# Kernel tuning notes

Measured on AMD Instinct MI355X. Metric: run time of the kernel, lower is better.

## Reference

```python
import jax, jax.numpy as jnp
import numpy as np

N, NFEAT, K, HK = 500000, 64, 8, 64

def _trunc_normal(key, shape, std):
    # torch.nn.init.trunc_normal_ truncates at +/-2 (then scaled by std)
    return jnp.clip(jax.random.normal(key, shape), -2.0, 2.0) * std

def setup_inputs() -> dict:
    key = jax.random.key(0)
    kx, kz, kt = jax.random.split(key, 3)
    x = jax.random.normal(kx, (N, NFEAT), dtype=jnp.float32)
    # stacked ParameterList: z[i] in R^{h_K x n}, t[i] in R^{h_K}
    z = _trunc_normal(kz, (K, HK, NFEAT), 1.0).astype(jnp.float32)  # b_z = 1.0
    t = _trunc_normal(kt, (K, HK), 1.0).astype(jnp.float32)         # b_t = 1.0
    return {"x": x, "z": z, "t": t}

def reference(x, z, t):
    w = jnp.exp(z)                                  # [K, HK, n], positive weights
    g = jnp.einsum('ni,khi->nkh', x, w) + t         # [N, K, HK]
    max_vals = jnp.max(g, axis=2)                   # [N, K] maxout per group
    max_idx = jnp.argmax(g, axis=2)                 # [N, K]
    y = jnp.min(max_vals, axis=1)                   # [N]   min over groups
    min_idx = jnp.argmin(max_vals, axis=1)          # [N]
    # A[min_idx[n], max_idx[n, min_idx[n]]] += 1  (vectorized scatter-add)
    cols = jnp.take_along_axis(max_idx, min_idx[:, None], axis=1)[:, 0]  # [N]
    A = jnp.zeros((K, HK), dtype=jnp.float32).at[min_idx, cols].add(1.0)
    return y, A
```

## Files before the change

kernel.cpp:

```cpp
#include <hip/hip_runtime.h>
#include <math.h>

constexpr int NS    = 500000;
constexpr int NF    = 64;
constexpr int KG    = 8;
constexpr int HKC   = 64;
constexpr int NCELL = KG * HKC;
constexpr int RPW   = 32;
constexpr int RPB   = 128;
constexpr int NBLK  = (NS + RPB - 1) / RPB;
constexpr int NSLOT = 1954;
constexpr int SLICE = HKC * NF;

typedef __attribute__((ext_vector_type(8))) _Float16 half8;
typedef __attribute__((ext_vector_type(4))) float f32x4;

__device__ __forceinline__ float swz16_f(float v) {
    return __int_as_float(__builtin_amdgcn_ds_swizzle(__float_as_int(v), 0x401F));
}
__device__ __forceinline__ int swz16_i(int v) {
    return __builtin_amdgcn_ds_swizzle(v, 0x401F);
}

__global__ void prep_kernel(const float* __restrict__ z,
                            _Float16* __restrict__ w_hi,
                            _Float16* __restrict__ w_lo,
                            float* __restrict__ A,
                            float4* __restrict__ pzero, int n4) {
    int i = blockIdx.x * blockDim.x + threadIdx.x;
    if (i < KG * HKC * NF) {
        float w = expf(z[i]);
        _Float16 h = (_Float16)w;
        w_hi[i] = h;
        w_lo[i] = (_Float16)(w - (float)h);
    }
    if (i < NCELL) A[i] = 0.0f;
    for (int j = i; j < n4; j += gridDim.x * blockDim.x)
        pzero[j] = (float4){0.f, 0.f, 0.f, 0.f};
}

template <bool PRIV>
__global__ __launch_bounds__(256, 3) void monn_mfma_kernel(
    const float* __restrict__ x,
    const _Float16* __restrict__ w_hi,
    const _Float16* __restrict__ w_lo,
    const float* __restrict__ t,
    float* __restrict__ y,
    float* __restrict__ dest) {

    __shared__ __align__(16) char smem[2 * 8192];
    __shared__ unsigned lhist[NCELL];
    if (PRIV) {
        for (int i = threadIdx.x; i < NCELL; i += 256) lhist[i] = 0u;
    }

    const int tid  = threadIdx.x;
    const int lane = tid & 63;
    const long base  = (long)blockIdx.x * RPB + (tid >> 6) * RPW;
    const bool valid = (base < NS);
    const long cbase = valid ? base : (NS - RPW);
    const int m  = lane & 15;
    const int q  = lane >> 4;
    const int q4 = q * 4;
    const int a32 = ((lane ^ 32) << 2);
    const int x7  = m & 7;
    const int rb0 = m * 128 + (((0 + q) ^ x7) << 4);
    const int rb1 = m * 128 + (((4 + q) ^ x7) << 4);
    const int sr  = tid >> 2;
    const int sc  = (tid & 3) * 2;
    const int sd0 = sr * 128 + (((sc)     ^ (sr & 7)) << 4);
    const int sd1 = sr * 128 + (((sc + 1) ^ (sr & 7)) << 4);

    half8 Xh[2][2], Xl[2][2];
#pragma unroll
    for (int rt = 0; rt < 2; ++rt) {
        const float* xp = x + (cbase + rt * 16 + m) * NF;
#pragma unroll
        for (int s = 0; s < 2; ++s) {
            const int k0 = s * 32 + q * 8;
            const float4 v0 = *reinterpret_cast<const float4*>(xp + k0);
            const float4 v1 = *reinterpret_cast<const float4*>(xp + k0 + 4);
            const float f[8] = {v0.x, v0.y, v0.z, v0.w, v1.x, v1.y, v1.z, v1.w};
#pragma unroll
            for (int j = 0; j < 8; ++j) {
                _Float16 h = (_Float16)f[j];
                Xh[rt][s][j] = h;
                Xl[rt][s][j] = (_Float16)(f[j] - (float)h);
            }
        }
    }

    float ymin[2] = {INFINITY, INFINITY};
    int   code[2] = {0, 0};

#pragma unroll 1
    for (int g = 0; g < KG; ++g) {
        __syncthreads();
        {
            const float4* sh = reinterpret_cast<const float4*>(w_hi + (size_t)g * SLICE);
            const float4* sl = reinterpret_cast<const float4*>(w_lo + (size_t)g * SLICE);
            const float4 h0 = sh[tid * 2], h1 = sh[tid * 2 + 1];
            const float4 l0 = sl[tid * 2], l1 = sl[tid * 2 + 1];
            *reinterpret_cast<float4*>(smem + sd0)        = h0;
            *reinterpret_cast<float4*>(smem + sd1)        = h1;
            *reinterpret_cast<float4*>(smem + 8192 + sd0) = l0;
            *reinterpret_cast<float4*>(smem + 8192 + sd1) = l1;
        }
        __syncthreads();

        f32x4 acc[4][2];
#pragma unroll
        for (int c = 0; c < 4; ++c) {
            const float4 tv = *reinterpret_cast<const float4*>(t + g * HKC + c * 16 + q4);
            const f32x4 tin = (f32x4){tv.x, tv.y, tv.z, tv.w};
            acc[c][0] = tin;
            acc[c][1] = tin;
        }

#pragma unroll
        for (int s = 0; s < 2; ++s) {
            const int rb = s ? rb1 : rb0;
            half8 Wh[4], Wl[4];
#pragma unroll
            for (int c = 0; c < 4; ++c) {
                Wh[c] = *reinterpret_cast<const half8*>(smem + rb + c * 2048);
                Wl[c] = *reinterpret_cast<const half8*>(smem + 8192 + rb + c * 2048);
            }
#pragma unroll
            for (int c = 0; c < 4; ++c)
#pragma unroll
                for (int rt = 0; rt < 2; ++rt)
                    acc[c][rt] = __builtin_amdgcn_mfma_f32_16x16x32_f16(Wh[c], Xh[rt][s], acc[c][rt], 0, 0, 0);
#pragma unroll
            for (int c = 0; c < 4; ++c)
#pragma unroll
                for (int rt = 0; rt < 2; ++rt)
                    acc[c][rt] = __builtin_amdgcn_mfma_f32_16x16x32_f16(Wl[c], Xh[rt][s], acc[c][rt], 0, 0, 0);
#pragma unroll
            for (int c = 0; c < 4; ++c)
#pragma unroll
                for (int rt = 0; rt < 2; ++rt)
                    acc[c][rt] = __builtin_amdgcn_mfma_f32_16x16x32_f16(Wh[c], Xl[rt][s], acc[c][rt], 0, 0, 0);
        }

#pragma unroll
        for (int rt = 0; rt < 2; ++rt) {
            float t01 = fmaxf(acc[0][rt][0], acc[0][rt][1]);
            float t23 = fmaxf(acc[0][rt][2], acc[0][rt][3]);
            float t45 = fmaxf(acc[1][rt][0], acc[1][rt][1]);
            float t67 = fmaxf(acc[1][rt][2], acc[1][rt][3]);
            float t89 = fmaxf(acc[2][rt][0], acc[2][rt][1]);
            float tab = fmaxf(acc[2][rt][2], acc[2][rt][3]);
            float tcd = fmaxf(acc[3][rt][0], acc[3][rt][1]);
            float tef = fmaxf(acc[3][rt][2], acc[3][rt][3]);
            float v = fmaxf(fmaxf(fmaxf(t01, t23), fmaxf(t45, t67)),
                            fmaxf(fmaxf(t89, tab), fmaxf(tcd, tef)));
            int h = 0;
#pragma unroll
            for (int c = 3; c >= 0; --c)
#pragma unroll
                for (int j = 3; j >= 0; --j)
                    h = (acc[c][rt][j] == v) ? (c * 16 + j) : h;
            h |= q4;
            {
                float v2 = swz16_f(v);
                int   h2 = swz16_i(h);
                bool take = (v2 > v) || (v2 == v && h2 < h);
                v = take ? v2 : v;  h = take ? h2 : h;
                float v3 = __int_as_float(__builtin_amdgcn_ds_bpermute(a32, __float_as_int(v)));
                int   h3 = __builtin_amdgcn_ds_bpermute(a32, h);
                take = (v3 > v) || (v3 == v && h3 < h);
                v = take ? v3 : v;  h = take ? h3 : h;
            }
            const bool better = v < ymin[rt];
            ymin[rt] = fminf(ymin[rt], v);
            code[rt] = better ? ((g << 6) | h) : code[rt];
        }
    }

    if (valid && q == 0) {
#pragma unroll
        for (int rt = 0; rt < 2; ++rt) {
            y[base + rt * 16 + m] = ymin[rt];
            if (PRIV) atomicAdd(&lhist[code[rt]], 1u);
            else      atomicAdd(&dest[code[rt]], 1.0f);
        }
    }

    if (PRIV) {
        __syncthreads();
        float* p = dest + (size_t)(blockIdx.x >> 1) * NCELL;
        for (int i = threadIdx.x; i < NCELL; i += 256) {
            const unsigned c = lhist[i];
            if (c) atomicAdd(&p[i], (float)c);
        }
    }
}

__global__ void reduce_kernel(const float* __restrict__ partial, float* __restrict__ A) {
    const int tid = blockIdx.x * blockDim.x + threadIdx.x;
    const int c = tid & (NCELL - 1);
    const int s = tid >> 9;
    float sum = 0.0f;
    for (int b = s; b < NSLOT; b += 32)
        sum += partial[(size_t)b * NCELL + c];
    atomicAdd(&A[c], sum);
}

extern "C" void kernel_launch(void* const* d_in, const int* in_sizes, int n_in,
                              void* d_out, int out_size, void* d_ws, size_t ws_size,
                              hipStream_t stream) {
    const float* x = (const float*)d_in[0];
    const float* z = (const float*)d_in[1];
    const float* t = (const float*)d_in[2];

    float* y = (float*)d_out;
    float* A = (float*)d_out + NS;

    _Float16* w_hi = (_Float16*)d_ws;
    _Float16* w_lo = w_hi + (size_t)KG * HKC * NF;
    float* partial = (float*)((char*)d_ws + 2 * sizeof(_Float16) * KG * HKC * NF);

    const size_t need = 2 * sizeof(_Float16) * KG * HKC * NF
                      + (size_t)NSLOT * NCELL * sizeof(float);

    const bool priv = (ws_size >= need);
    const int n4 = priv ? (NSLOT * NCELL / 4) : 0;

    prep_kernel<<<1024, 256, 0, stream>>>(z, w_hi, w_lo, A, (float4*)partial, n4);

    if (priv) {
        monn_mfma_kernel<true><<<NBLK, 256, 0, stream>>>(x, w_hi, w_lo, t, y, partial);
        reduce_kernel<<<64, 256, 0, stream>>>(partial, A);
    } else {
        monn_mfma_kernel<false><<<NBLK, 256, 0, stream>>>(x, w_hi, w_lo, t, y, A);
    }
}
```

Measured before the change: 266.2 us.

## Make MFMA kernel persistent with all weights resident in LDS

Replaces the one-block-per-128-rows launch with 256 persistent 1024-thread blocks. Each block loads all 8 weight groups (hi and lo fp16, 128 KB) plus t into LDS once, then loops over 32-row tiles with no per-group barriers or reloads. Histogram counts collect in a per-block LDS histogram and are flushed with global atomics, which removes the partial-buffer zeroing and the reduce kernel. In exchange, LDS use rises to about 130 KB per block, so only one block fits per CU. The launch bound of 4 may not be reachable, and 256 blocks may not fill every CU.

```diff
diff --git a/kernel.cpp b/kernel.cpp
--- a/kernel.cpp
+++ b/kernel.cpp
@@ -7,9 +7,10 @@
 constexpr int HKC   = 64;
 constexpr int NCELL = KG * HKC;
 constexpr int RPW   = 32;
-constexpr int RPB   = 128;
-constexpr int NBLK  = (NS + RPB - 1) / RPB;
-constexpr int NSLOT = 1954;
+constexpr int TPB   = 1024;
+constexpr int NBLK  = 256;
+constexpr int NTILE = NS / RPW;
+constexpr int NWAVES = NBLK * (TPB / 64);
 constexpr int SLICE = HKC * NF;
 
 typedef __attribute__((ext_vector_type(8))) _Float16 half8;
@@ -25,8 +26,7 @@
 __global__ void prep_kernel(const float* __restrict__ z,
                             _Float16* __restrict__ w_hi,
                             _Float16* __restrict__ w_lo,
-                            float* __restrict__ A,
-                            float4* __restrict__ pzero, int n4) {
+                            float* __restrict__ A) {
     int i = blockIdx.x * blockDim.x + threadIdx.x;
     if (i < KG * HKC * NF) {
         float w = expf(z[i]);
@@ -35,30 +35,42 @@
         w_lo[i] = (_Float16)(w - (float)h);
     }
     if (i < NCELL) A[i] = 0.0f;
-    for (int j = i; j < n4; j += gridDim.x * blockDim.x)
-        pzero[j] = (float4){0.f, 0.f, 0.f, 0.f};
-}
-
-template <bool PRIV>
-__global__ __launch_bounds__(256, 3) void monn_mfma_kernel(
+}
+
+__global__ __launch_bounds__(TPB, 4) void monn_mfma_kernel(
     const float* __restrict__ x,
     const _Float16* __restrict__ w_hi,
     const _Float16* __restrict__ w_lo,
     const float* __restrict__ t,
     float* __restrict__ y,
-    float* __restrict__ dest) {
-
-    __shared__ __align__(16) char smem[2 * 8192];
+    float* __restrict__ A) {
+
+    __shared__ __align__(16) char smem[2 * KG * 8192];
+    __shared__ __align__(16) float t_lds[KG * HKC];
     __shared__ unsigned lhist[NCELL];
-    if (PRIV) {
-        for (int i = threadIdx.x; i < NCELL; i += 256) lhist[i] = 0u;
-    }
-
-    const int tid  = threadIdx.x;
+
+    const int tid = threadIdx.x;
+
+    {
+        const float4* sh = reinterpret_cast<const float4*>(w_hi);
+        const float4* sl = reinterpret_cast<const float4*>(w_lo);
+#pragma unroll
+        for (int i = 0; i < 4; ++i) {
+            const int ci  = i * 1024 + tid;
+            const int row = (ci >> 3) & 63;
+            const int ch  = ci & 7;
+            const int addr = (ci >> 9) * 8192 + row * 128 + ((ch ^ (row & 7)) << 4);
+            *reinterpret_cast<float4*>(smem + addr)         = sh[ci];
+            *reinterpret_cast<float4*>(smem + 65536 + addr) = sl[ci];
+        }
+        if (tid < 128)
+            reinterpret_cast<float4*>(t_lds)[tid] =
+                reinterpret_cast<const float4*>(t)[tid];
+        if (tid < NCELL) lhist[tid] = 0u;
+    }
+    __syncthreads();
+
     const int lane = tid & 63;
-    const long base  = (long)blockIdx.x * RPB + (tid >> 6) * RPW;
-    const bool valid = (base < NS);
-    const long cbase = valid ? base : (NS - RPW);
     const int m  = lane & 15;
     const int q  = lane >> 4;
     const int q4 = q * 4;
@@ -66,145 +78,120 @@
     const int x7  = m & 7;
     const int rb0 = m * 128 + (((0 + q) ^ x7) << 4);
     const int rb1 = m * 128 + (((4 + q) ^ x7) << 4);
-    const int sr  = tid >> 2;
-    const int sc  = (tid & 3) * 2;
-    const int sd0 = sr * 128 + (((sc)     ^ (sr & 7)) << 4);
-    const int sd1 = sr * 128 + (((sc + 1) ^ (sr & 7)) << 4);
-
-    half8 Xh[2][2], Xl[2][2];
-#pragma unroll
-    for (int rt = 0; rt < 2; ++rt) {
-        const float* xp = x + (cbase + rt * 16 + m) * NF;
-#pragma unroll
-        for (int s = 0; s < 2; ++s) {
-            const int k0 = s * 32 + q * 8;
-            const float4 v0 = *reinterpret_cast<const float4*>(xp + k0);
-            const float4 v1 = *reinterpret_cast<const float4*>(xp + k0 + 4);
-            const float f[8] = {v0.x, v0.y, v0.z, v0.w, v1.x, v1.y, v1.z, v1.w};
-#pragma unroll
-            for (int j = 0; j < 8; ++j) {
-                _Float16 h = (_Float16)f[j];
-                Xh[rt][s][j] = h;
-                Xl[rt][s][j] = (_Float16)(f[j] - (float)h);
-            }
-        }
-    }
-
-    float ymin[2] = {INFINITY, INFINITY};
-    int   code[2] = {0, 0};
+    const int gwave = blockIdx.x * (TPB / 64) + (tid >> 6);
 
 #pragma unroll 1
-    for (int g = 0; g < KG; ++g) {
-        __syncthreads();
-        {
-            const float4* sh = reinterpret_cast<const float4*>(w_hi + (size_t)g * SLICE);
-            const float4* sl = reinterpret_cast<const float4*>(w_lo + (size_t)g * SLICE);
-            const float4 h0 = sh[tid * 2], h1 = sh[tid * 2 + 1];
-            const float4 l0 = sl[tid * 2], l1 = sl[tid * 2 + 1];
-            *reinterpret_cast<float4*>(smem + sd0)        = h0;
-            *reinterpret_cast<float4*>(smem + sd1)        = h1;
-            *reinterpret_cast<float4*>(smem + 8192 + sd0) = l0;
-            *reinterpret_cast<float4*>(smem + 8192 + sd1) = l1;
-        }
-        __syncthreads();
-
-        f32x4 acc[4][2];
-#pragma unroll
-        for (int c = 0; c < 4; ++c) {
-            const float4 tv = *reinterpret_cast<const float4*>(t + g * HKC + c * 16 + q4);
-            const f32x4 tin = (f32x4){tv.x, tv.y, tv.z, tv.w};
-            acc[c][0] = tin;
-            acc[c][1] = tin;
-        }
-
-#pragma unroll
-        for (int s = 0; s < 2; ++s) {
-            const int rb = s ? rb1 : rb0;
-            half8 Wh[4], Wl[4];
+    for (int tile = gwave; tile < NTILE; tile += NWAVES) {
+        const long base = (long)tile * RPW;
+
+        half8 Xh[2][2], Xl[2][2];
+#pragma unroll
+        for (int rt = 0; rt < 2; ++rt) {
+            const float* xp = x + (base + rt * 16 + m) * NF;
+#pragma unroll
+            for (int s = 0; s < 2; ++s) {
+                const int k0 = s * 32 + q * 8;
+                const float4 v0 = *reinterpret_cast<const float4*>(xp + k0);
+                const float4 v1 = *reinterpret_cast<const float4*>(xp + k0 + 4);
+                const float f[8] = {v0.x, v0.y, v0.z, v0.w, v1.x, v1.y, v1.z, v1.w};
+#pragma unroll
+                for (int j = 0; j < 8; ++j) {
+                    _Float16 h = (_Float16)f[j];
+                    Xh[rt][s][j] = h;
+                    Xl[rt][s][j] = (_Float16)(f[j] - (float)h);
+                }
+            }
+        }
+
+        float ymin[2] = {INFINITY, INFINITY};
+        int   code[2] = {0, 0};
+
+#pragma unroll 1
+        for (int g = 0; g < KG; ++g) {
+            f32x4 acc[4][2];
 #pragma unroll
             for (int c = 0; c < 4; ++c) {
-                Wh[c] = *reinterpret_cast<const half8*>(smem + rb + c * 2048);
-                Wl[c] = *reinterpret_cast<const half8*>(smem + 8192 + rb + c * 2048);
-            }
-#pragma unroll
-            for (int c = 0; c < 4; ++c)
-#pragma unroll
-                for (int rt = 0; rt < 2; ++rt)
-                    acc[c][rt] = __builtin_amdgcn_mfma_f32_16x16x32_f16(Wh[c], Xh[rt][s], acc[c][rt], 0, 0, 0);
-#pragma unroll
-            for (int c = 0; c < 4; ++c)
-#pragma unroll
-                for (int rt = 0; rt < 2; ++rt)
-                    acc[c][rt] = __builtin_amdgcn_mfma_f32_16x16x32_f16(Wl[c], Xh[rt][s], acc[c][rt], 0, 0, 0);
-#pragma unroll
-            for (int c = 0; c < 4; ++c)
-#pragma unroll
-                for (int rt = 0; rt < 2; ++rt)
-                    acc[c][rt] = __builtin_amdgcn_mfma_f32_16x16x32_f16(Wh[c], Xl[rt][s], acc[c][rt], 0, 0, 0);
-        }
-
-#pragma unroll
-        for (int rt = 0; rt < 2; ++rt) {
-            float t01 = fmaxf(acc[0][rt][0], acc[0][rt][1]);
-            float t23 = fmaxf(acc[0][rt][2], acc[0][rt][3]);
-            float t45 = fmaxf(acc[1][rt][0], acc[1][rt][1]);
-            float t67 = fmaxf(acc[1][rt][2], acc[1][rt][3]);
-            float t89 = fmaxf(acc[2][rt][0], acc[2][rt][1]);
-            float tab = fmaxf(acc[2][rt][2], acc[2][rt][3]);
-            float tcd = fmaxf(acc[3][rt][0], acc[3][rt][1]);
-            float tef = fmaxf(acc[3][rt][2], acc[3][rt][3]);
-            float v = fmaxf(fmaxf(fmaxf(t01, t23), fmaxf(t45, t67)),
-                            fmaxf(fmaxf(t89, tab), fmaxf(tcd, tef)));
-            int h = 0;
-#pragma unroll
-            for (int c = 3; c >= 0; --c)
-#pragma unroll
-                for (int j = 3; j >= 0; --j)
-                    h = (acc[c][rt][j] == v) ? (c * 16 + j) : h;
-            h |= q4;
-            {
-                float v2 = swz16_f(v);
-                int   h2 = swz16_i(h);
-                bool take = (v2 > v) || (v2 == v && h2 < h);
-                v = take ? v2 : v;  h = take ? h2 : h;
-                float v3 = __int_as_float(__builtin_amdgcn_ds_bpermute(a32, __float_as_int(v)));
-                int   h3 = __builtin_amdgcn_ds_bpermute(a32, h);
-                take = (v3 > v) || (v3 == v && h3 < h);
-                v = take ? v3 : v;  h = take ? h3 : h;
-            }
-            const bool better = v < ymin[rt];
-            ymin[rt] = fminf(ymin[rt], v);
-            code[rt] = better ? ((g << 6) | h) : code[rt];
-        }
-    }
-
-    if (valid && q == 0) {
-#pragma unroll
-        for (int rt = 0; rt < 2; ++rt) {
-            y[base + rt * 16 + m] = ymin[rt];
-            if (PRIV) atomicAdd(&lhist[code[rt]], 1u);
-            else      atomicAdd(&dest[code[rt]], 1.0f);
-        }
-    }
-
-    if (PRIV) {
-        __syncthreads();
-        float* p = dest + (size_t)(blockIdx.x >> 1) * NCELL;
-        for (int i = threadIdx.x; i < NCELL; i += 256) {
-            const unsigned c = lhist[i];
-            if (c) atomicAdd(&p[i], (float)c);
-        }
-    }
-}
-
-__global__ void reduce_kernel(const float* __restrict__ partial, float* __restrict__ A) {
-    const int tid = blockIdx.x * blockDim.x + threadIdx.x;
-    const int c = tid & (NCELL - 1);
-    const int s = tid >> 9;
-    float sum = 0.0f;
-    for (int b = s; b < NSLOT; b += 32)
-        sum += partial[(size_t)b * NCELL + c];
-    atomicAdd(&A[c], sum);
+                const float4 tv = *reinterpret_cast<const float4*>(
+                    t_lds + g * HKC + c * 16 + q4);
+                acc[c][0] = (f32x4){tv.x, tv.y, tv.z, tv.w};
+                acc[c][1] = acc[c][0];
+            }
+
+#pragma unroll
+            for (int s = 0; s < 2; ++s) {
+                const int rb = (s ? rb1 : rb0) + g * 8192;
+                half8 Wh[4], Wl[4];
+#pragma unroll
+                for (int c = 0; c < 4; ++c) {
+                    Wh[c] = *reinterpret_cast<const half8*>(smem + rb + c * 2048);
+                    Wl[c] = *reinterpret_cast<const half8*>(smem + 65536 + rb + c * 2048);
+                }
+#pragma unroll
+                for (int c = 0; c < 4; ++c)
+#pragma unroll
+                    for (int rt = 0; rt < 2; ++rt)
+                        acc[c][rt] = __builtin_amdgcn_mfma_f32_16x16x32_f16(Wh[c], Xh[rt][s], acc[c][rt], 0, 0, 0);
+#pragma unroll
+                for (int c = 0; c < 4; ++c)
+#pragma unroll
+                    for (int rt = 0; rt < 2; ++rt)
+                        acc[c][rt] = __builtin_amdgcn_mfma_f32_16x16x32_f16(Wl[c], Xh[rt][s], acc[c][rt], 0, 0, 0);
+#pragma unroll
+                for (int c = 0; c < 4; ++c)
+#pragma unroll
+                    for (int rt = 0; rt < 2; ++rt)
+                        acc[c][rt] = __builtin_amdgcn_mfma_f32_16x16x32_f16(Wh[c], Xl[rt][s], acc[c][rt], 0, 0, 0);
+            }
+
+#pragma unroll
+            for (int rt = 0; rt < 2; ++rt) {
+                float t01 = fmaxf(acc[0][rt][0], acc[0][rt][1]);
+                float t23 = fmaxf(acc[0][rt][2], acc[0][rt][3]);
+                float t45 = fmaxf(acc[1][rt][0], acc[1][rt][1]);
+                float t67 = fmaxf(acc[1][rt][2], acc[1][rt][3]);
+                float t89 = fmaxf(acc[2][rt][0], acc[2][rt][1]);
+                float tab = fmaxf(acc[2][rt][2], acc[2][rt][3]);
+                float tcd = fmaxf(acc[3][rt][0], acc[3][rt][1]);
+                float tef = fmaxf(acc[3][rt][2], acc[3][rt][3]);
+                float v = fmaxf(fmaxf(fmaxf(t01, t23), fmaxf(t45, t67)),
+                                fmaxf(fmaxf(t89, tab), fmaxf(tcd, tef)));
+                int h = 0;
+#pragma unroll
+                for (int c = 3; c >= 0; --c)
+#pragma unroll
+                    for (int j = 3; j >= 0; --j)
+                        h = (acc[c][rt][j] == v) ? (c * 16 + j) : h;
+                h |= q4;
+                {
+                    float v2 = swz16_f(v);
+                    int   h2 = swz16_i(h);
+                    bool take = (v2 > v) || (v2 == v && h2 < h);
+                    v = take ? v2 : v;  h = take ? h2 : h;
+                    float v3 = __int_as_float(__builtin_amdgcn_ds_bpermute(a32, __float_as_int(v)));
+                    int   h3 = __builtin_amdgcn_ds_bpermute(a32, h);
+                    take = (v3 > v) || (v3 == v && h3 < h);
+                    v = take ? v3 : v;  h = take ? h3 : h;
+                }
+                const bool better = v < ymin[rt];
+                ymin[rt] = fminf(ymin[rt], v);
+                code[rt] = better ? ((g << 6) | h) : code[rt];
+            }
+        }
+
+        if (q == 0) {
+#pragma unroll
+            for (int rt = 0; rt < 2; ++rt) {
+                y[base + rt * 16 + m] = ymin[rt];
+                atomicAdd(&lhist[code[rt]], 1u);
+            }
+        }
+    }
+
+    __syncthreads();
+    for (int i = tid; i < NCELL; i += TPB) {
+        const unsigned c = lhist[i];
+        if (c) atomicAdd(&A[i], (float)c);
+    }
 }
 
 extern "C" void kernel_launch(void* const* d_in, const int* in_sizes, int n_in,
@@ -219,20 +206,7 @@
 
     _Float16* w_hi = (_Float16*)d_ws;
     _Float16* w_lo = w_hi + (size_t)KG * HKC * NF;
-    float* partial = (float*)((char*)d_ws + 2 * sizeof(_Float16) * KG * HKC * NF);
-
-    const size_t need = 2 * sizeof(_Float16) * KG * HKC * NF
-                      + (size_t)NSLOT * NCELL * sizeof(float);
-
-    const bool priv = (ws_size >= need);
-    const int n4 = priv ? (NSLOT * NCELL / 4) : 0;
-
-    prep_kernel<<<1024, 256, 0, stream>>>(z, w_hi, w_lo, A, (float4*)partial, n4);
-
-    if (priv) {
-        monn_mfma_kernel<true><<<NBLK, 256, 0, stream>>>(x, w_hi, w_lo, t, y, partial);
-        reduce_kernel<<<64, 256, 0, stream>>>(partial, A);
-    } else {
-        monn_mfma_kernel<false><<<NBLK, 256, 0, stream>>>(x, w_hi, w_lo, t, y, A);
-    }
-}
+
+    prep_kernel<<<128, 256, 0, stream>>>(z, w_hi, w_lo, A);
+    monn_mfma_kernel<<<NBLK, TPB, 0, stream>>>(x, w_hi, w_lo, t, y, A);
+}
```

After: 230.7 us. 1.15x faster.
